# Performance work log

Hardware: AMD Instinct MI355X
Metric: run time of the kernel (lower is better)

Reference implementation:

```python
import jax, jax.numpy as jnp
import numpy as np

D_MODEL = 1024
NUM_HEADS = 16
SEQ_LEN = 2048
BATCH = 2
THETA = 10000.0


def apply_rope(x, positions, theta=THETA):
    # x: [b, h, s, d]; positions: [s] int
    d = x.shape[-1]
    inv_freq = 1.0 / (theta ** (jnp.arange(0, d, 2, dtype=jnp.float32) / d))  # [d/2]
    ang = positions.astype(jnp.float32)[:, None] * inv_freq[None, :]  # [s, d/2]
    cos, sin = jnp.cos(ang), jnp.sin(ang)  # [s, d/2]
    x_even = x[..., 0::2]
    x_odd = x[..., 1::2]
    out_even = x_even * cos - x_odd * sin
    out_odd = x_even * sin + x_odd * cos
    # re-interleave pairs
    out = jnp.stack([out_even, out_odd], axis=-1).reshape(x.shape)
    return out


def setup_inputs() -> dict:
    key = jax.random.key(0)
    ks = jax.random.split(key, 5)
    scale = 1.0 / np.sqrt(D_MODEL)
    return {
        "in_features": jax.random.normal(ks[0], (BATCH, SEQ_LEN, D_MODEL), dtype=jnp.float32),
        "token_positions": jnp.arange(SEQ_LEN, dtype=jnp.int32),
        "q_w": jax.random.normal(ks[1], (D_MODEL, D_MODEL), dtype=jnp.float32) * scale,
        "k_w": jax.random.normal(ks[2], (D_MODEL, D_MODEL), dtype=jnp.float32) * scale,
        "v_w": jax.random.normal(ks[3], (D_MODEL, D_MODEL), dtype=jnp.float32) * scale,
        "o_w": jax.random.normal(ks[4], (D_MODEL, D_MODEL), dtype=jnp.float32) * scale,
    }


def reference(in_features, token_positions, q_w, k_w, v_w, o_w):
    b, s, _ = in_features.shape
    h = NUM_HEADS
    d_k = D_MODEL // h

    # Linear stores weights [out, in]: y = x @ W^T
    def proj(x, w):
        y = jnp.einsum('bsi,oi->bso', x, w)
        return y.reshape(b, s, h, d_k).transpose(0, 2, 1, 3)  # [b, h, s, d]

    q = apply_rope(proj(in_features, q_w), token_positions)
    k = apply_rope(proj(in_features, k_w), token_positions)
    v = proj(in_features, v_w)

    scores = jnp.einsum('bhqd,bhkd->bhqk', q, k) / jnp.sqrt(jnp.float32(d_k))
    causal = jnp.tril(jnp.ones((s, s), dtype=bool))
    scores = jnp.where(causal, scores, jnp.float32(-1e30))
    attn = jax.nn.softmax(scores, axis=-1)
    out = jnp.einsum('bhqk,bhkd->bhqd', attn, v)  # [b, h, s, d]
    out = out.transpose(0, 2, 1, 3).reshape(b, s, h * d_k)
    return jnp.einsum('bsi,oi->bso', out, o_w)
```

## Files before the change

kernel.cpp:

```cpp
#include <hip/hip_runtime.h>
#include <hip/hip_bf16.h>

typedef unsigned short ushort_t;
typedef unsigned int uint_t;
typedef __attribute__((ext_vector_type(4))) float f32x4;
typedef __attribute__((ext_vector_type(16))) float f32x16;
typedef __attribute__((ext_vector_type(8))) short short8;
typedef __attribute__((ext_vector_type(4))) short short4x;
typedef __attribute__((ext_vector_type(4))) unsigned short u16x4;
typedef __attribute__((ext_vector_type(2))) uint_t u32x2;

typedef const __attribute__((address_space(1))) unsigned char glob_t;
typedef __attribute__((address_space(3))) unsigned char lds_t;

#define S_LEN 2048
#define DM 1024
#define NH 16
#define DH 64
#define NB 2
#define BH (NB*NH)
#define MROWS (NB*S_LEN)

#define SCALE_L2E 0.18033688f

__device__ __forceinline__ float bf2f(ushort_t u) {
    return __uint_as_float(((uint_t)u) << 16);
}
__device__ __forceinline__ ushort_t f2bf(float f) {
    __hip_bfloat16 h = __float2bfloat16(f);
    return *reinterpret_cast<ushort_t*>(&h);
}

__global__ __launch_bounds__(256) void prep_all(
    const float* __restrict__ X,  const float* __restrict__ Wq,
    const float* __restrict__ Wk, const float* __restrict__ Wv,
    const float* __restrict__ Wo, const int* __restrict__ pos,
    ushort_t* __restrict__ Xb,  ushort_t* __restrict__ Wqb,
    ushort_t* __restrict__ Wkb, ushort_t* __restrict__ Wvb,
    ushort_t* __restrict__ Wob, float2* __restrict__ tab)
{
    int bid = blockIdx.x;
    if (bid < 8192) {
        size_t i = (size_t)bid * 256 + threadIdx.x;
        size_t e = i * 4;
        const float* src; ushort_t* dst; size_t off;
        if (e < (size_t)MROWS * DM) { src = X; dst = Xb; off = e; }
        else {
            size_t r = e - (size_t)MROWS * DM;
            int w = (int)(r >> 20); off = r & 1048575;
            src = (w == 0) ? Wq : (w == 1) ? Wk : (w == 2) ? Wv : Wo;
            dst = (w == 0) ? Wqb : (w == 1) ? Wkb : (w == 2) ? Wvb : Wob;
        }
        float4 v = *reinterpret_cast<const float4*>(src + off);
        u16x4 o;
        o[0] = f2bf(v.x); o[1] = f2bf(v.y); o[2] = f2bf(v.z); o[3] = f2bf(v.w);
        *reinterpret_cast<u16x4*>(dst + off) = o;
    } else {
        int i = (bid - 8192) * 256 + threadIdx.x;
        int s = i >> 5, f = i & 31;
        float inv = powf(10000.0f, -(float)f / 32.0f);
        float ang = (float)pos[s] * inv;
        tab[i] = make_float2(cosf(ang), sinf(ang));
    }
}

template<int MODE>
__global__ __launch_bounds__(256) void gemm128b(
    const ushort_t* __restrict__ A,
    const ushort_t* __restrict__ W0, const ushort_t* __restrict__ W1,
    const ushort_t* __restrict__ W2,
    ushort_t* __restrict__ D0, ushort_t* __restrict__ D1,
    ushort_t* __restrict__ D2,
    float* __restrict__ Fout, const float2* __restrict__ tab)
{
    __shared__ __attribute__((aligned(16))) ushort_t As[128 * 32];
    __shared__ __attribute__((aligned(16))) ushort_t Bs[128 * 32];
    const ushort_t* W = (MODE == 1 || blockIdx.z == 0) ? W0
                        : (blockIdx.z == 1 ? W1 : W2);
    ushort_t* Dst = (blockIdx.z == 0) ? D0 : (blockIdx.z == 1) ? D1 : D2;
    int m0 = blockIdx.x * 128, n0 = blockIdx.y * 128;
    int tid = threadIdx.x, lane = tid & 63, wv = tid >> 6;
    int wm = wv >> 1, wn = wv & 1;
    int l15 = lane & 15, g = lane >> 4;

    f32x4 acc[4][4];
    for (int i = 0; i < 4; i++)
        for (int j = 0; j < 4; j++)
            acc[i][j] = (f32x4){0.f, 0.f, 0.f, 0.f};

    int srow = wv * 32 + (lane >> 2);
    int scol = (lane & 3) * 8;
    const ushort_t* Ap = A + (size_t)(m0 + srow) * DM + scol;
    const ushort_t* Wp = W + (size_t)(n0 + srow) * DM + scol;
    lds_t* laA0 = (lds_t*)&As[wv * 1024];
    lds_t* laA1 = (lds_t*)&As[wv * 1024 + 512];
    lds_t* laB0 = (lds_t*)&Bs[wv * 1024];
    lds_t* laB1 = (lds_t*)&Bs[wv * 1024 + 512];

    for (int kk = 0; kk < DM; kk += 32) {
        __builtin_amdgcn_global_load_lds((glob_t*)(Ap + kk), laA0, 16, 0, 0);
        __builtin_amdgcn_global_load_lds((glob_t*)(Ap + 16 * DM + kk), laA1, 16, 0, 0);
        __builtin_amdgcn_global_load_lds((glob_t*)(Wp + kk), laB0, 16, 0, 0);
        __builtin_amdgcn_global_load_lds((glob_t*)(Wp + 16 * DM + kk), laB1, 16, 0, 0);
        __syncthreads();
        short8 af[4], bf[4];
        for (int i = 0; i < 4; i++)
            af[i] = *reinterpret_cast<const short8*>(
                &As[(wm * 64 + i * 16 + l15) * 32 + g * 8]);
        for (int j = 0; j < 4; j++)
            bf[j] = *reinterpret_cast<const short8*>(
                &Bs[(wn * 64 + j * 16 + l15) * 32 + g * 8]);
        __builtin_amdgcn_s_setprio(1);
        for (int i = 0; i < 4; i++)
            for (int j = 0; j < 4; j++)
                acc[i][j] = __builtin_amdgcn_mfma_f32_16x16x32_bf16(
                    af[i], bf[j], acc[i][j], 0, 0, 0);
        __builtin_amdgcn_s_setprio(0);
        __syncthreads();
    }

    for (int i = 0; i < 4; i++) {
        for (int j = 0; j < 4; j++) {
            int mbase = m0 + wm * 64 + i * 16 + g * 4;
            int n = n0 + wn * 64 + j * 16 + l15;
            if (MODE == 0) {
                int h = n >> 6, d = n & 63;
                if (blockIdx.z < 2) {
                    int f = d >> 1;
                    float sgn = (d & 1) ? 1.f : -1.f;
                    float sc = (blockIdx.z == 0) ? SCALE_L2E : 1.0f;
                    for (int r = 0; r < 4; r++) {
                        int m = mbase + r;
                        int b = m >> 11, s = m & 2047;
                        float v = acc[i][j][r];
                        float p = __shfl_xor(v, 1);
                        float2 cs = tab[s * 32 + f];
                        float out = (v * cs.x + p * cs.y * sgn) * sc;
                        Dst[(((size_t)(b * NH + h)) * S_LEN + s) * DH + d] =
                            f2bf(out);
                    }
                } else {
                    for (int r = 0; r < 4; r++) {
                        int m = mbase + r;
                        int b = m >> 11, s = m & 2047;
                        Dst[((size_t)(b * NH + h) * DH + d) * S_LEN + s] =
                            f2bf(acc[i][j][r]);
                    }
                }
            } else {
                for (int r = 0; r < 4; r++)
                    Fout[(size_t)(mbase + r) * DM + n] = acc[i][j][r];
            }
        }
    }
}

#define WAITV0 asm volatile("s_waitcnt vmcnt(0)" ::: "memory")

__global__ __launch_bounds__(512, 4) void attn_k15(
    const ushort_t* __restrict__ Q, const ushort_t* __restrict__ K,
    const ushort_t* __restrict__ Vt, ushort_t* __restrict__ O)
{
    __shared__ __attribute__((aligned(16))) ushort_t Ks[2][8192];
    __shared__ __attribute__((aligned(16))) ushort_t Vs[2][8192];

    int tid = threadIdx.x, wv = tid >> 6, lane = tid & 63;
    int l31 = lane & 31, h = lane >> 5, r7 = l31 & 7;
    int bid = blockIdx.x;
    int u = (bid < 256) ? (15 - (bid >> 5)) : ((bid - 256) >> 5);
    int bh = bid & 31;
    int qsub = wv & 3, hf = wv >> 2;
    int qmin = u * 128 + qsub * 32, qmax = qmin + 31;
    int ntr = u + 1;

    const ushort_t* Qp = Q + (size_t)bh * S_LEN * DH;
    const char* Kp = (const char*)(K + (size_t)bh * S_LEN * DH);
    const char* Vp = (const char*)(Vt + (size_t)bh * DH * S_LEN);

    short8 qf[4];
    {
        const ushort_t* qp = Qp + (((size_t)(qmin + l31)) << 6) + h * 8;
        #pragma unroll
        for (int ds = 0; ds < 4; ds++)
            qf[ds] = *reinterpret_cast<const short8*>(qp + ds * 16);
    }

    f32x16 oacc[2];
    oacc[0] = (f32x16){0.f};
    oacc[1] = (f32x16){0.f};
    float m_run = -1e20f, l_run = 0.f;

#define STAGE16(buf, kk0) do {                                                \
    _Pragma("unroll") for (int c_ = 0; c_ < 2; ++c_) {                        \
        int L_ = c_ * 8192 + tid * 16;                                        \
        int rk_ = L_ >> 7;                                                    \
        int ck_ = (L_ & 127) ^ ((rk_ & 7) << 4);                              \
        __builtin_amdgcn_global_load_lds(                                     \
            (glob_t*)(Kp + (size_t)((kk0) + rk_) * 128 + ck_),                \
            (lds_t*)((char*)&Ks[buf][0] + c_ * 8192 + wv * 1024), 16, 0, 0);  \
        int rv_ = L_ >> 8;                                                    \
        int cb_ = L_ & 255;                                                   \
        int cv_ = ((cb_ & 127) ^ ((rv_ & 7) << 4)) | (cb_ & 128);             \
        __builtin_amdgcn_global_load_lds(                                     \
            (glob_t*)(Vp + (size_t)rv_ * (S_LEN * 2) + (size_t)(kk0) * 2      \
                      + cv_),                                                 \
            (lds_t*)((char*)&Vs[buf][0] + c_ * 8192 + wv * 1024), 16, 0, 0);  \
    } } while (0)

    STAGE16(0, 0);
    WAITV0;
    __builtin_amdgcn_s_barrier();

    int buf = 0;
    for (int t = 0; t < ntr; ++t) {
        if (t + 1 < ntr) STAGE16(buf ^ 1, (t + 1) * 128);

        int k0 = t * 128 + hf * 64;
        if (k0 <= qmax) {
            const char* kb = (const char*)&Ks[buf][0];
            const char* vbp = (const char*)&Vs[buf][0];

            f32x16 st[2];
            #pragma unroll
            for (int s = 0; s < 2; s++) {
                short8 kf[4];
                #pragma unroll
                for (int ds = 0; ds < 4; ds++)
                    kf[ds] = *reinterpret_cast<const short8*>(
                        kb + (hf * 64 + s * 32 + l31) * 128
                        + (((h + 2 * ds) ^ r7) << 4));
                __builtin_amdgcn_s_setprio(1);
                f32x16 z = {0.f};
                #pragma unroll
                for (int ds = 0; ds < 4; ds++)
                    z = __builtin_amdgcn_mfma_f32_32x32x16_bf16(
                        kf[ds], qf[ds], z, 0, 0, 0);
                st[s] = z;
                __builtin_amdgcn_s_setprio(0);
            }

            if (k0 + 63 > qmin) {
                int q = qmin + l31;
                #pragma unroll
                for (int s = 0; s < 2; s++)
                    #pragma unroll
                    for (int r = 0; r < 16; r++)
                        if ((k0 + s * 32 + (r & 3) + 8 * (r >> 2) + 4 * h) > q)
                            st[s][r] = -1e30f;
            }

            if (t == 0) {
                float m0v = st[0][0], m1v = st[1][0];
                #pragma unroll
                for (int r = 1; r < 16; r++) {
                    m0v = fmaxf(m0v, st[0][r]);
                    m1v = fmaxf(m1v, st[1][r]);
                }
                float m16 = fmaxf(m0v, m1v);
                m16 = fmaxf(m16, __shfl_xor(m16, 32));
                m_run = m16 + 8.0f;
            }

            float ps = 0.f;
            short4x pa[2][4];
            #pragma unroll
            for (int s = 0; s < 2; s++)
                #pragma unroll
                for (int kt = 0; kt < 4; kt++) {
                    float p0 = exp2f(st[s][4 * kt + 0] - m_run);
                    float p1 = exp2f(st[s][4 * kt + 1] - m_run);
                    float p2 = exp2f(st[s][4 * kt + 2] - m_run);
                    float p3 = exp2f(st[s][4 * kt + 3] - m_run);
                    ps += (p0 + p1) + (p2 + p3);
                    u32x2 w = { (uint_t)f2bf(p0) | ((uint_t)f2bf(p1) << 16),
                                (uint_t)f2bf(p2) | ((uint_t)f2bf(p3) << 16) };
                    pa[s][kt] = __builtin_bit_cast(short4x, w);
                }
            l_run += ps;

            #pragma unroll
            for (int s = 0; s < 2; s++) {
                short4x vb[2][4];
                #pragma unroll
                for (int db = 0; db < 2; db++)
                    #pragma unroll
                    for (int kt = 0; kt < 4; kt++) {
                        int c = s * 4 + kt;
                        vb[db][kt] = *reinterpret_cast<const short4x*>(
                            vbp + (db * 32 + l31) * 256 + hf * 128
                            + (((c ^ r7) & 7) << 4) + h * 8);
                    }
                __builtin_amdgcn_s_setprio(1);
                #pragma unroll
                for (int kt = 0; kt < 4; kt++) {
                    oacc[0] = __builtin_amdgcn_mfma_f32_32x32x8bf16_1k(
                        vb[0][kt], pa[s][kt], oacc[0], 0, 0, 0);
                    oacc[1] = __builtin_amdgcn_mfma_f32_32x32x8bf16_1k(
                        vb[1][kt], pa[s][kt], oacc[1], 0, 0, 0);
                }
                __builtin_amdgcn_s_setprio(0);
            }
        }

        WAITV0;
        __builtin_amdgcn_s_barrier();
        buf ^= 1;
    }

    {
        float* smK = (float*)&Ks[0][0];
        float* smV = (float*)&Vs[0][0];
        float* base = (qsub < 2) ? smK : smV;
        float* slot = base + ((qsub & 1) * 64 + lane) * 34;
        if (hf == 1) {
            #pragma unroll
            for (int j = 0; j < 16; j++) slot[j] = oacc[0][j];
            #pragma unroll
            for (int j = 0; j < 16; j++) slot[16 + j] = oacc[1][j];
            slot[32] = l_run;
            slot[33] = m_run;
        }
        __syncthreads();
        if (hf == 0) {
            float lB = slot[32], mB = slot[33];
            float ms = fmaxf(m_run, mB);
            float fa = exp2f(m_run - ms), fb = exp2f(mB - ms);
            float l_tot = l_run * fa + lB * fb;
            l_tot += __shfl_xor(l_tot, 32);
            float inv = 1.0f / l_tot;
            int b = bh >> 4, head = bh & 15;
            int q_row = qmin + l31;
            size_t obase = ((size_t)b * S_LEN + q_row) * DM + head * DH;
            #pragma unroll
            for (int db = 0; db < 2; db++)
                #pragma unroll
                for (int rg = 0; rg < 4; rg++) {
                    u16x4 o;
                    #pragma unroll
                    for (int j = 0; j < 4; j++) {
                        float v = oacc[db][rg * 4 + j] * fa
                                + slot[db * 16 + rg * 4 + j] * fb;
                        o[j] = f2bf(v * inv);
                    }
                    *reinterpret_cast<u16x4*>(
                        &O[obase + db * 32 + rg * 8 + h * 4]) = o;
                }
        }
    }
#undef STAGE16
}

extern "C" void kernel_launch(void* const* d_in, const int* in_sizes, int n_in,
                              void* d_out, int out_size, void* d_ws, size_t ws_size,
                              hipStream_t stream)
{
    const float* X  = (const float*)d_in[0];
    const int* pos  = (const int*)d_in[1];
    const float* qw = (const float*)d_in[2];
    const float* kw = (const float*)d_in[3];
    const float* vw = (const float*)d_in[4];
    const float* ow = (const float*)d_in[5];
    float* out = (float*)d_out;

    char* ws = (char*)d_ws;
    ushort_t* Xb   = (ushort_t*)(ws);
    ushort_t* Wqb  = (ushort_t*)(ws + 8388608);
    ushort_t* Wkb  = (ushort_t*)(ws + 10485760);
    ushort_t* Wvb  = (ushort_t*)(ws + 12582912);
    ushort_t* Wob  = (ushort_t*)(ws + 14680064);
    ushort_t* Qbh  = (ushort_t*)(ws + 16777216);
    ushort_t* Kbh  = (ushort_t*)(ws + 25165824);
    ushort_t* Vtb  = (ushort_t*)(ws + 41943040);
    ushort_t* AttO = (ushort_t*)(ws + 50331648);
    float2*   tab  = (float2*)(ws + 58720256);

    prep_all<<<8448, 256, 0, stream>>>(X, qw, kw, vw, ow, pos,
                                       Xb, Wqb, Wkb, Wvb, Wob, tab);
    gemm128b<0><<<dim3(32, 8, 3), 256, 0, stream>>>(
        Xb, Wqb, Wkb, Wvb, Qbh, Kbh, Vtb, nullptr, tab);
    attn_k15<<<512, 512, 0, stream>>>(Qbh, Kbh, Vtb, AttO);
    gemm128b<1><<<dim3(32, 8, 1), 256, 0, stream>>>(
        AttO, Wob, nullptr, nullptr, nullptr, nullptr, nullptr, out, tab);
}
```

Measured before the change: 119.4 us.

## Replace QKV projection with 256x256-tile pipelined GEMM over concatenated weights

Adds a new 512-thread QKV GEMM kernel using 256x256 output tiles, a 64-wide K step, swizzled LDS with direct global-to-LDS loads, double buffering split into four phases with setprio around MFMA bursts, and a RoPE/scale/transpose epilogue. It treats Wq, Wk and Wv as one contiguous 3072-row weight matrix, which relies on their being adjacent in the workspace. The change aims to raise data reuse per tile and overlap loads with MFMA compared with the older 128x128 kernel. The trade-off is a larger tile that gives only 192 blocks, which may underfill the GPU, plus higher register and LDS pressure.

```diff
diff --git a/kernel.cpp b/kernel.cpp
--- a/kernel.cpp
+++ b/kernel.cpp
@@ -30,6 +30,9 @@
     __hip_bfloat16 h = __float2bfloat16(f);
     return *reinterpret_cast<ushort_t*>(&h);
 }
+
+#define WAITV0 asm volatile("s_waitcnt vmcnt(0)" ::: "memory")
+#define WAITV2 asm volatile("s_waitcnt vmcnt(2)" ::: "memory")
 
 __global__ __launch_bounds__(256) void prep_all(
     const float* __restrict__ X,  const float* __restrict__ Wq,
@@ -64,6 +67,141 @@
     }
 }
 
+__global__ __launch_bounds__(512, 2) void qkv8_gemm(
+    const ushort_t* __restrict__ A, const ushort_t* __restrict__ W3,
+    ushort_t* __restrict__ Qd, ushort_t* __restrict__ Kd,
+    ushort_t* __restrict__ Vtd, const float2* __restrict__ tab)
+{
+    __shared__ __attribute__((aligned(16))) ushort_t As[2][2][8192];
+    __shared__ __attribute__((aligned(16))) ushort_t Bs[2][2][8192];
+
+    int tid = threadIdx.x, wv = tid >> 6, lane = tid & 63;
+    int l15 = lane & 15, g = lane >> 4;
+    int wm = wv >> 2, wn = wv & 3, wbh = wn >> 1;
+    int m0 = blockIdx.x * 256, n0 = blockIdx.y * 256;
+    int swz = (l15 & 7) << 4;
+    const char* Ab = (const char*)A;
+    const char* Wb = (const char*)W3;
+
+    f32x4 acc[8][4];
+    #pragma unroll
+    for (int i = 0; i < 8; i++)
+        #pragma unroll
+        for (int j = 0; j < 4; j++)
+            acc[i][j] = (f32x4){0.f, 0.f, 0.f, 0.f};
+
+#define STG_A(hh, t) do {                                                     \
+    _Pragma("unroll") for (int c_ = 0; c_ < 2; ++c_) {                        \
+        int L_ = c_ * 8192 + tid * 16;                                        \
+        int row_ = L_ >> 7;                                                   \
+        int cb_ = (L_ & 127) ^ ((row_ & 7) << 4);                             \
+        __builtin_amdgcn_global_load_lds(                                     \
+            (glob_t*)(Ab + ((size_t)(m0 + (hh) * 128 + row_) * DM             \
+                      + (t) * 64) * 2 + cb_),                                 \
+            (lds_t*)((char*)&As[hh][(t) & 1][0] + c_ * 8192 + wv * 1024),     \
+            16, 0, 0);                                                        \
+    } } while (0)
+#define STG_B(hh, t) do {                                                     \
+    _Pragma("unroll") for (int c_ = 0; c_ < 2; ++c_) {                        \
+        int L_ = c_ * 8192 + tid * 16;                                        \
+        int row_ = L_ >> 7;                                                   \
+        int cb_ = (L_ & 127) ^ ((row_ & 7) << 4);                             \
+        __builtin_amdgcn_global_load_lds(                                     \
+            (glob_t*)(Wb + ((size_t)(n0 + (hh) * 128 + row_) * DM             \
+                      + (t) * 64) * 2 + cb_),                                 \
+            (lds_t*)((char*)&Bs[hh][(t) & 1][0] + c_ * 8192 + wv * 1024),     \
+            16, 0, 0);                                                        \
+    } } while (0)
+
+    short8 bf[4][2];
+#define DO_PHASE(t, q, STAGES, WCNT) do {                                     \
+    const char* ab_ = (const char*)&As[wm][(t) & 1][0];                       \
+    const char* bb_ = (const char*)&Bs[wbh][(t) & 1][0];                      \
+    if ((q) == 0) {                                                           \
+        _Pragma("unroll") for (int j_ = 0; j_ < 4; ++j_)                      \
+        _Pragma("unroll") for (int ks_ = 0; ks_ < 2; ++ks_)                   \
+            bf[j_][ks_] = *reinterpret_cast<const short8*>(                   \
+                bb_ + ((wn & 1) * 64 + j_ * 16 + l15) * 128                   \
+                + ((ks_ * 64 + g * 16) ^ swz));                               \
+    }                                                                         \
+    short8 af_[2][2];                                                         \
+    _Pragma("unroll") for (int ii_ = 0; ii_ < 2; ++ii_)                       \
+    _Pragma("unroll") for (int ks_ = 0; ks_ < 2; ++ks_)                       \
+        af_[ii_][ks_] = *reinterpret_cast<const short8*>(                     \
+            ab_ + (((q) * 2 + ii_) * 16 + l15) * 128                          \
+            + ((ks_ * 64 + g * 16) ^ swz));                                   \
+    STAGES;                                                                   \
+    __builtin_amdgcn_s_barrier();                                             \
+    __builtin_amdgcn_s_setprio(1);                                            \
+    _Pragma("unroll") for (int ii_ = 0; ii_ < 2; ++ii_)                       \
+    _Pragma("unroll") for (int j_ = 0; j_ < 4; ++j_)                          \
+    _Pragma("unroll") for (int ks_ = 0; ks_ < 2; ++ks_)                       \
+        acc[(q) * 2 + ii_][j_] = __builtin_amdgcn_mfma_f32_16x16x32_bf16(     \
+            af_[ii_][ks_], bf[j_][ks_], acc[(q) * 2 + ii_][j_], 0, 0, 0);     \
+    __builtin_amdgcn_s_setprio(0);                                            \
+    WCNT;                                                                     \
+    __builtin_amdgcn_s_barrier();                                             \
+} while (0)
+
+    STG_A(0, 0); STG_A(1, 0);
+    STG_B(0, 0); STG_B(1, 0);
+    STG_B(0, 1); STG_B(1, 1);
+    WAITV0;
+    __builtin_amdgcn_s_barrier();
+
+    for (int I = 0; I < 8; ++I) {
+        int T = 2 * I;
+        bool more = (I < 7);
+        DO_PHASE(T, 0, { STG_A(0, T + 1); }, {});
+        DO_PHASE(T, 1, { STG_A(1, T + 1); if (more) STG_B(0, T + 2); }, {});
+        DO_PHASE(T, 2, { if (more) STG_B(1, T + 2); }, {});
+        DO_PHASE(T, 3, {}, { if (more) { WAITV2; } else { WAITV0; } });
+        DO_PHASE(T + 1, 0, { if (more) STG_A(0, T + 2); }, {});
+        DO_PHASE(T + 1, 1, { if (more) { STG_A(1, T + 2); STG_B(0, T + 3); } }, {});
+        DO_PHASE(T + 1, 2, { if (more) STG_B(1, T + 3); }, {});
+        DO_PHASE(T + 1, 3, {}, { if (more) { WAITV2; } else { WAITV0; } });
+    }
+    WAITV0;
+
+    #pragma unroll
+    for (int i = 0; i < 8; i++) {
+        #pragma unroll
+        for (int j = 0; j < 4; j++) {
+            int mb = m0 + wm * 128 + i * 16 + g * 4;
+            int n = n0 + wn * 64 + j * 16 + l15;
+            int w = n >> 10, rem = n & 1023;
+            int hh = rem >> 6, d = rem & 63;
+            if (w < 2) {
+                int f = d >> 1;
+                float sgn = (d & 1) ? 1.f : -1.f;
+                float sc = (w == 0) ? SCALE_L2E : 1.0f;
+                ushort_t* Dst = (w == 0) ? Qd : Kd;
+                #pragma unroll
+                for (int r = 0; r < 4; r++) {
+                    int m = mb + r;
+                    int b = m >> 11, s = m & 2047;
+                    float v = acc[i][j][r];
+                    float p = __shfl_xor(v, 1);
+                    float2 cs = tab[s * 32 + f];
+                    Dst[(((size_t)(b * NH + hh)) * S_LEN + s) * DH + d] =
+                        f2bf((v * cs.x + p * cs.y * sgn) * sc);
+                }
+            } else {
+                #pragma unroll
+                for (int r = 0; r < 4; r++) {
+                    int m = mb + r;
+                    int b = m >> 11, s = m & 2047;
+                    Vtd[((size_t)(b * NH + hh) * DH + d) * S_LEN + s] =
+                        f2bf(acc[i][j][r]);
+                }
+            }
+        }
+    }
+#undef DO_PHASE
+#undef STG_A
+#undef STG_B
+}
+
 template<int MODE>
 __global__ __launch_bounds__(256) void gemm128b(
     const ushort_t* __restrict__ A,
@@ -155,8 +293,6 @@
     }
 }
 
-#define WAITV0 asm volatile("s_waitcnt vmcnt(0)" ::: "memory")
-
 __global__ __launch_bounds__(512, 4) void attn_k15(
     const ushort_t* __restrict__ Q, const ushort_t* __restrict__ K,
     const ushort_t* __restrict__ Vt, ushort_t* __restrict__ O)
@@ -376,8 +512,8 @@
 
     prep_all<<<8448, 256, 0, stream>>>(X, qw, kw, vw, ow, pos,
                                        Xb, Wqb, Wkb, Wvb, Wob, tab);
-    gemm128b<0><<<dim3(32, 8, 3), 256, 0, stream>>>(
-        Xb, Wqb, Wkb, Wvb, Qbh, Kbh, Vtb, nullptr, tab);
+    qkv8_gemm<<<dim3(16, 12), 512, 0, stream>>>(
+        Xb, Wqb, Qbh, Kbh, Vtb, tab);
     attn_k15<<<512, 512, 0, stream>>>(Qbh, Kbh, Vtb, AttO);
     gemm128b<1><<<dim3(32, 8, 1), 256, 0, stream>>>(
         AttO, Wob, nullptr, nullptr, nullptr, nullptr, nullptr, out, tab);
```

After: 125.4 us. 1.05x slower.
